# Kernel tuning notes

Hardware: AMD Instinct MI355X
Metric: run time of the kernel (lower is better)

Reference implementation:

```python
import math
import jax, jax.numpy as jnp
import numpy as np

HEAD_DIM = 128
SKETCH_DIM = 256  # multiple of 8, no padding needed in pack
_BIT_WEIGHTS = jnp.array([1, 2, 4, 8, 16, 32, 64, 128], dtype=jnp.uint8)


def _pack_bits(bits):
    # bits: uint8 0/1, trailing dim = SKETCH_DIM (multiple of 8)
    *lead, d = bits.shape
    b = bits.reshape(*lead, d // 8, 8)
    return (b * _BIT_WEIGHTS).sum(axis=-1).astype(jnp.uint8)


def _unpack_bits(packed, out_dim):
    # packed: uint8 [..., n] -> float32 [..., out_dim] of 0/1
    shifts = jnp.arange(8, dtype=jnp.uint8)
    bits = (packed[..., None] >> shifts) & jnp.uint8(1)
    bits = bits.reshape(*packed.shape[:-1], -1)[..., :out_dim]
    return bits.astype(jnp.float32)


def setup_inputs() -> dict:
    key = jax.random.key(0)
    kq, kk, kg = jax.random.split(key, 3)
    q = jax.random.normal(kq, (4, 32, 16, HEAD_DIM), dtype=jnp.float32)
    k = jax.random.normal(kk, (4, 32, 8192, HEAD_DIM), dtype=jnp.float32)
    G = jax.random.normal(kg, (HEAD_DIM, SKETCH_DIM), dtype=jnp.float32) / math.sqrt(SKETCH_DIM)
    return {"q": q, "k": k, "G": G}


def reference(q, k, G):
    # project_query: q @ G -> [B, H, Q, sketch_dim]
    q_sketch = jnp.einsum('bhqd,ds->bhqs', q, G)
    # sketch_key: sign-quantize k @ G, pack into uint8
    proj = jnp.einsum('bhkd,ds->bhks', k, G)
    bits = (proj > 0).astype(jnp.uint8)
    k_packed = _pack_bits(bits)  # [B, H, K, sketch_dim//8] uint8
    # estimate_scores: unpack to +/-1, dequant matmul, unbiasing scale
    k_signs = _unpack_bits(k_packed, SKETCH_DIM) * 2.0 - 1.0
    est = jnp.einsum('bhqs,bhks->bhqk', q_sketch, k_signs.astype(q_sketch.dtype))
    return est * jnp.float32(math.sqrt(math.pi / 2))
```

## Files before the change

### kernel.cpp

```cpp
#include <hip/hip_runtime.h>
#include <math.h>

typedef _Float16 f16;
typedef _Float16 f16x8 __attribute__((ext_vector_type(8)));
typedef float    f32x4 __attribute__((ext_vector_type(4)));
typedef unsigned int u32;
typedef unsigned long long u64;

#define NHEADS 128
#define KLEN   8192
#define DDIM   128
#define SDIM   256
#define NROWS  (NHEADS * KLEN)
#define SCALE  1.2533141373155003f
#define TAU    2e-5f

#define QS_OFF     0
#define GH_OFF     (1u << 20)
#define GL_OFF     ((1u << 20) + (64u << 10))
#define GT_OFF     ((1u << 20) + (128u << 10))
#define PACKED_OFF (2u << 20)

__device__ __forceinline__ float seq_dot_np(const float* __restrict__ a,
                                            const float* __restrict__ gcol) {
  float acc = 0.0f;
  #pragma unroll 8
  for (int d = 0; d < DDIM; ++d)
    acc = __builtin_fmaf(a[d], gcol[d], acc);
  return acc;
}

__global__ void prep_qs_kernel(const float* __restrict__ q,
                               const float* __restrict__ G,
                               f16* __restrict__ qs16) {
  int idx = blockIdx.x * 256 + threadIdx.x;
  int s  = idx & 255;
  int hq = idx >> 8;
  const float* qr = q + (size_t)hq * DDIM;
  float acc = 0.f;
  #pragma unroll 8
  for (int d = 0; d < DDIM; ++d) acc += qr[d] * G[d * SDIM + s];
  qs16[idx] = (f16)acc;
}

__global__ void prep_g_kernel(const float* __restrict__ G,
                              f16* __restrict__ gh, f16* __restrict__ gl,
                              float* __restrict__ gt) {
  int idx = blockIdx.x * 256 + threadIdx.x;
  int d = idx & 127;
  int s = idx >> 7;
  float g = G[d * SDIM + s];
  f16 h = (f16)g;
  gh[s * DDIM + d] = h;
  gl[s * DDIM + d] = (f16)((g - (float)h) * 4096.0f);
  gt[s * DDIM + d] = g;
}

__launch_bounds__(1024)
__global__ void proj_sign_kernel(const float* __restrict__ kmat,
                                 const f16* __restrict__ gh,
                                 const f16* __restrict__ gl,
                                 u32* __restrict__ packed,
                                 u32* __restrict__ smask) {
  __shared__ __align__(16) char smem[131072];

  const int tid  = threadIdx.x;
  const int lane = tid & 63;
  const int w    = tid >> 6;
  const int g4 = lane >> 4;
  const int ln = lane & 15;

  #pragma unroll
  for (int j = 0; j < 4; ++j) {
    int cidx = j * 1024 + tid;
    int s = cidx >> 4;
    int off = (cidx * 16) ^ ((s & 7) << 4);
    *(f16x8*)(smem + off)         = *(const f16x8*)(gh + (size_t)cidx * 8);
    *(f16x8*)(smem + 65536 + off) = *(const f16x8*)(gl + (size_t)cidx * 8);
  }
  __syncthreads();

  const int base = blockIdx.x * 512 + w * 32;

  f16x8 Ah[2][4], Al[2][4];
  #pragma unroll
  for (int rb = 0; rb < 2; ++rb) {
    const float* kr = kmat + (size_t)(base + rb * 16 + ln) * DDIM;
    #pragma unroll
    for (int c = 0; c < 4; ++c) {
      const float* p0 = kr + c * 32 + g4 * 8;
      float4 a0 = *(const float4*)p0;
      float4 a1 = *(const float4*)(p0 + 4);
      float af[8] = {a0.x, a0.y, a0.z, a0.w, a1.x, a1.y, a1.z, a1.w};
      f16x8 hh, ll;
      #pragma unroll
      for (int j = 0; j < 8; ++j) {
        f16 h = (f16)af[j];
        hh[j] = h;
        ll[j] = (f16)((af[j] - (float)h) * 4096.0f);
      }
      Ah[rb][c] = hh;
      Al[rb][c] = ll;
    }
  }

  u32 pw[2][8] = {{0}};
  u32 sw[2][8] = {{0}};

  #pragma unroll
  for (int tl = 0; tl < 16; ++tl) {
    const int s = tl * 16 + ln;
    const int sx = (s & 7) << 4;
    f16x8 Bh[4], Bl[4];
    #pragma unroll
    for (int c = 0; c < 4; ++c) {
      int off = (s * 256 + c * 64 + g4 * 16) ^ sx;
      Bh[c] = *(const f16x8*)(smem + off);
      Bl[c] = *(const f16x8*)(smem + 65536 + off);
    }
    f32x4 ah0 = {0,0,0,0}, aa0 = {0,0,0,0}, ab0 = {0,0,0,0};
    f32x4 ah1 = {0,0,0,0}, aa1 = {0,0,0,0}, ab1 = {0,0,0,0};
    #pragma unroll
    for (int c = 0; c < 4; ++c) {
      ah0 = __builtin_amdgcn_mfma_f32_16x16x32_f16(Ah[0][c], Bh[c], ah0, 0, 0, 0);
      aa0 = __builtin_amdgcn_mfma_f32_16x16x32_f16(Ah[0][c], Bl[c], aa0, 0, 0, 0);
      ab0 = __builtin_amdgcn_mfma_f32_16x16x32_f16(Al[0][c], Bh[c], ab0, 0, 0, 0);
      ah1 = __builtin_amdgcn_mfma_f32_16x16x32_f16(Ah[1][c], Bh[c], ah1, 0, 0, 0);
      aa1 = __builtin_amdgcn_mfma_f32_16x16x32_f16(Ah[1][c], Bl[c], aa1, 0, 0, 0);
      ab1 = __builtin_amdgcn_mfma_f32_16x16x32_f16(Al[1][c], Bh[c], ab1, 0, 0, 0);
    }
    float p[2][4];
    #pragma unroll
    for (int r = 0; r < 4; ++r) {
      p[0][r] = ah0[r] + (aa0[r] + ab0[r]) * 2.44140625e-4f;
      p[1][r] = ah1[r] + (aa1[r] + ab1[r]) * 2.44140625e-4f;
    }

    #pragma unroll
    for (int rb = 0; rb < 2; ++rb) {
      u64 b0 = __ballot(p[rb][0] > 0.0f ? 1 : 0);
      u64 b1 = __ballot(p[rb][1] > 0.0f ? 1 : 0);
      u64 b2 = __ballot(p[rb][2] > 0.0f ? 1 : 0);
      u64 b3 = __ballot(p[rb][3] > 0.0f ? 1 : 0);
      if (lane < 16) {
        int r = lane & 3;
        u64 b = (r == 0) ? b0 : (r == 1) ? b1 : (r == 2) ? b2 : b3;
        u32 sh = 16u * (u32)(lane >> 2);
        pw[rb][tl >> 1] |= ((u32)((b >> sh) & 0xffffu)) << (16 * (tl & 1));
      }
    }

    float mn = __builtin_fabsf(p[0][0]);
    #pragma unroll
    for (int rb = 0; rb < 2; ++rb)
      #pragma unroll
      for (int r = 0; r < 4; ++r)
        mn = fminf(mn, __builtin_fabsf(p[rb][r]));
    if (__any(mn < TAU ? 1 : 0)) {
      #pragma unroll
      for (int rb = 0; rb < 2; ++rb) {
        u64 t0 = __ballot(__builtin_fabsf(p[rb][0]) < TAU ? 1 : 0);
        u64 t1 = __ballot(__builtin_fabsf(p[rb][1]) < TAU ? 1 : 0);
        u64 t2 = __ballot(__builtin_fabsf(p[rb][2]) < TAU ? 1 : 0);
        u64 t3 = __ballot(__builtin_fabsf(p[rb][3]) < TAU ? 1 : 0);
        if (lane < 16) {
          int r = lane & 3;
          u64 t = (r == 0) ? t0 : (r == 1) ? t1 : (r == 2) ? t2 : t3;
          u32 sh = 16u * (u32)(lane >> 2);
          sw[rb][tl >> 1] |= ((u32)((t >> sh) & 0xffffu)) << (16 * (tl & 1));
        }
      }
    }
  }

  if (lane < 16) {
    #pragma unroll
    for (int rb = 0; rb < 2; ++rb) {
      size_t row = (size_t)(base + rb * 16 + lane);
      uint4 v0, v1, m0, m1;
      v0.x = pw[rb][0]; v0.y = pw[rb][1]; v0.z = pw[rb][2]; v0.w = pw[rb][3];
      v1.x = pw[rb][4]; v1.y = pw[rb][5]; v1.z = pw[rb][6]; v1.w = pw[rb][7];
      m0.x = sw[rb][0]; m0.y = sw[rb][1]; m0.z = sw[rb][2]; m0.w = sw[rb][3];
      m1.x = sw[rb][4]; m1.y = sw[rb][5]; m1.z = sw[rb][6]; m1.w = sw[rb][7];
      *(uint4*)(packed + row * 8)     = v0;
      *(uint4*)(packed + row * 8 + 4) = v1;
      *(uint4*)(smask  + row * 8)     = m0;
      *(uint4*)(smask  + row * 8 + 4) = m1;
    }
  }
}

__global__ void fixup_kernel(const float* __restrict__ kmat,
                             const float* __restrict__ gt,
                             u32* __restrict__ packed,
                             const u32* __restrict__ smask) {
  int row = blockIdx.x * 256 + threadIdx.x;
  if (row >= NROWS) return;
  const u32* mp = smask + (size_t)row * 8;
  uint4 m0 = *(const uint4*)mp;
  uint4 m1 = *(const uint4*)(mp + 4);
  u32 mw[8] = {m0.x, m0.y, m0.z, m0.w, m1.x, m1.y, m1.z, m1.w};
  if (!(mw[0] | mw[1] | mw[2] | mw[3] | mw[4] | mw[5] | mw[6] | mw[7])) return;
  const float* a = kmat + (size_t)row * DDIM;
  #pragma unroll
  for (int wd = 0; wd < 8; ++wd) {
    u32 m = mw[wd];
    if (!m) continue;
    u32 pk = packed[(size_t)row * 8 + wd];
    while (m) {
      int b = __ffs(m) - 1;  m &= m - 1;
      int s = wd * 32 + b;
      float acc = seq_dot_np(a, gt + (size_t)s * DDIM);
      if (acc > 0.0f) pk |= (1u << b);
      else            pk &= ~(1u << b);
    }
    packed[(size_t)row * 8 + wd] = pk;
  }
}

__launch_bounds__(256)
__global__ void est_kernel(const f16* __restrict__ qs16,
                           const u32* __restrict__ packed,
                           float* __restrict__ out) {
  const int tid  = threadIdx.x;
  const int lane = tid & 63;
  const int w    = tid >> 6;
  const int wg   = blockIdx.x;
  const int head   = wg >> 5;
  const int kchunk = (wg & 31) * 256;
  const int g4 = lane >> 4, ln = lane & 15;

  f16x8 aq[8];
  const f16* qb = qs16 + (size_t)head * 16 * SDIM;
  #pragma unroll
  for (int c = 0; c < 8; ++c)
    aq[c] = *(const f16x8*)(qb + ln * SDIM + c * 32 + g4 * 8);

  const int kb = kchunk + w * 64;
  #pragma unroll
  for (int kt = 0; kt < 4; ++kt) {
    int krow = kb + kt * 16 + ln;
    const u32* bp = packed + (size_t)(head * KLEN + krow) * 8;
    uint4 q0 = *(const uint4*)bp;
    uint4 q1 = *(const uint4*)(bp + 4);
    u32 b32[8] = {q0.x, q0.y, q0.z, q0.w, q1.x, q1.y, q1.z, q1.w};
    f32x4 acc = {0, 0, 0, 0};
    #pragma unroll
    for (int c = 0; c < 8; ++c) {
      u32 byte8 = (b32[c] >> (8 * g4)) & 0xffu;
      union { u32 u[4]; f16x8 h; } sv;
      #pragma unroll
      for (int pp = 0; pp < 4; ++pp) {
        u32 v = 0x3C003C00u;
        v |= ((byte8 >> (2 * pp))     & 1u) ? 0u : 0x8000u;
        v |= ((byte8 >> (2 * pp + 1)) & 1u) ? 0u : 0x80000000u;
        sv.u[pp] = v;
      }
      acc = __builtin_amdgcn_mfma_f32_16x16x32_f16(aq[c], sv.h, acc, 0, 0, 0);
    }
    float* ob = out + (size_t)(head * 16) * KLEN + kb + kt * 16 + ln;
    #pragma unroll
    for (int r = 0; r < 4; ++r) {
      int qrow = g4 * 4 + r;
      ob[(size_t)qrow * KLEN] = acc[r] * SCALE;
    }
  }
}

extern "C" void kernel_launch(void* const* d_in, const int* in_sizes, int n_in,
                              void* d_out, int out_size, void* d_ws, size_t ws_size,
                              hipStream_t stream) {
  const float* q = (const float*)d_in[0];
  const float* k = (const float*)d_in[1];
  const float* G = (const float*)d_in[2];
  float* out = (float*)d_out;
  char* ws = (char*)d_ws;

  f16*   qs16   = (f16*)(ws + QS_OFF);
  f16*   gh     = (f16*)(ws + GH_OFF);
  f16*   gl     = (f16*)(ws + GL_OFF);
  float* gt     = (float*)(ws + GT_OFF);
  u32*   packed = (u32*)(ws + PACKED_OFF);

  u32* smask = (u32*)d_out;

  prep_qs_kernel<<<2048, 256, 0, stream>>>(q, G, qs16);
  prep_g_kernel<<<128, 256, 0, stream>>>(G, gh, gl, gt);
  proj_sign_kernel<<<2048, 1024, 0, stream>>>(k, gh, gl, packed, smask);
  fixup_kernel<<<4096, 256, 0, stream>>>(k, gt, packed, smask);
  est_kernel<<<4096, 256, 0, stream>>>(qs16, packed, out);
}
```

Measured before the change: 363.4 us.

## Read MFMA-fragment-ordered G directly from global memory instead of shared memory

The G prep kernel now writes the f16 hi/lo split of G already laid out in per-lane MFMA fragment order, so the projection kernel loads B fragments straight from global memory (L1/L2-resident, 128 KB) with coalesced 16-byte loads. This removes the per-block 128 KB shared-memory staging and its barrier, so blocks shrink to 256 threads over 128 rows and the grid grows fourfold. The trade-off is that every wave re-reads G through the cache hierarchy instead of from LDS, which may add L2 traffic and latency.

```diff
diff --git a/kernel.cpp b/kernel.cpp
--- a/kernel.cpp
+++ b/kernel.cpp
@@ -16,8 +16,8 @@
 #define TAU    2e-5f
 
 #define QS_OFF     0
-#define GH_OFF     (1u << 20)
-#define GL_OFF     ((1u << 20) + (64u << 10))
+#define GFH_OFF    (1u << 20)
+#define GFL_OFF    ((1u << 20) + (64u << 10))
 #define GT_OFF     ((1u << 20) + (128u << 10))
 #define PACKED_OFF (2u << 20)
 
@@ -44,43 +44,40 @@
 }
 
 __global__ void prep_g_kernel(const float* __restrict__ G,
-                              f16* __restrict__ gh, f16* __restrict__ gl,
+                              f16* __restrict__ gfh, f16* __restrict__ gfl,
                               float* __restrict__ gt) {
-  int idx = blockIdx.x * 256 + threadIdx.x;
-  int d = idx & 127;
-  int s = idx >> 7;
-  float g = G[d * SDIM + s];
-  f16 h = (f16)g;
-  gh[s * DDIM + d] = h;
-  gl[s * DDIM + d] = (f16)((g - (float)h) * 4096.0f);
-  gt[s * DDIM + d] = g;
-}
-
-__launch_bounds__(1024)
+  int t = blockIdx.x * 256 + threadIdx.x;
+  int tl   = t >> 8;
+  int c    = (t >> 6) & 3;
+  int lane = t & 63;
+  int s  = tl * 16 + (lane & 15);
+  int d0 = c * 32 + (lane >> 4) * 8;
+  f16x8 hh, ll;
+  #pragma unroll
+  for (int j = 0; j < 8; ++j) {
+    float g = G[(size_t)(d0 + j) * SDIM + s];
+    f16 h = (f16)g;
+    hh[j] = h;
+    ll[j] = (f16)((g - (float)h) * 4096.0f);
+    gt[(size_t)s * DDIM + d0 + j] = g;
+  }
+  *(f16x8*)(gfh + (size_t)t * 8) = hh;
+  *(f16x8*)(gfl + (size_t)t * 8) = ll;
+}
+
+__launch_bounds__(256)
 __global__ void proj_sign_kernel(const float* __restrict__ kmat,
-                                 const f16* __restrict__ gh,
-                                 const f16* __restrict__ gl,
+                                 const f16* __restrict__ gfh,
+                                 const f16* __restrict__ gfl,
                                  u32* __restrict__ packed,
                                  u32* __restrict__ smask) {
-  __shared__ __align__(16) char smem[131072];
-
   const int tid  = threadIdx.x;
   const int lane = tid & 63;
   const int w    = tid >> 6;
   const int g4 = lane >> 4;
   const int ln = lane & 15;
 
-  #pragma unroll
-  for (int j = 0; j < 4; ++j) {
-    int cidx = j * 1024 + tid;
-    int s = cidx >> 4;
-    int off = (cidx * 16) ^ ((s & 7) << 4);
-    *(f16x8*)(smem + off)         = *(const f16x8*)(gh + (size_t)cidx * 8);
-    *(f16x8*)(smem + 65536 + off) = *(const f16x8*)(gl + (size_t)cidx * 8);
-  }
-  __syncthreads();
-
-  const int base = blockIdx.x * 512 + w * 32;
+  const int base = blockIdx.x * 128 + w * 32;
 
   f16x8 Ah[2][4], Al[2][4];
   #pragma unroll
@@ -107,16 +104,16 @@
   u32 pw[2][8] = {{0}};
   u32 sw[2][8] = {{0}};
 
+  const size_t loff = (size_t)lane * 8;
+
   #pragma unroll
   for (int tl = 0; tl < 16; ++tl) {
-    const int s = tl * 16 + ln;
-    const int sx = (s & 7) << 4;
     f16x8 Bh[4], Bl[4];
     #pragma unroll
     for (int c = 0; c < 4; ++c) {
-      int off = (s * 256 + c * 64 + g4 * 16) ^ sx;
-      Bh[c] = *(const f16x8*)(smem + off);
-      Bl[c] = *(const f16x8*)(smem + 65536 + off);
+      size_t o = (size_t)(tl * 4 + c) * 512 + loff;
+      Bh[c] = *(const f16x8*)(gfh + o);
+      Bl[c] = *(const f16x8*)(gfl + o);
     }
     f32x4 ah0 = {0,0,0,0}, aa0 = {0,0,0,0}, ab0 = {0,0,0,0};
     f32x4 ah1 = {0,0,0,0}, aa1 = {0,0,0,0}, ab1 = {0,0,0,0};
@@ -277,16 +274,16 @@
   char* ws = (char*)d_ws;
 
   f16*   qs16   = (f16*)(ws + QS_OFF);
-  f16*   gh     = (f16*)(ws + GH_OFF);
-  f16*   gl     = (f16*)(ws + GL_OFF);
+  f16*   gfh    = (f16*)(ws + GFH_OFF);
+  f16*   gfl    = (f16*)(ws + GFL_OFF);
   float* gt     = (float*)(ws + GT_OFF);
   u32*   packed = (u32*)(ws + PACKED_OFF);
 
   u32* smask = (u32*)d_out;
 
   prep_qs_kernel<<<2048, 256, 0, stream>>>(q, G, qs16);
-  prep_g_kernel<<<128, 256, 0, stream>>>(G, gh, gl, gt);
-  proj_sign_kernel<<<2048, 1024, 0, stream>>>(k, gh, gl, packed, smask);
+  prep_g_kernel<<<16, 256, 0, stream>>>(G, gfh, gfl, gt);
+  proj_sign_kernel<<<8192, 256, 0, stream>>>(k, gfh, gfl, packed, smask);
   fixup_kernel<<<4096, 256, 0, stream>>>(k, gt, packed, smask);
   est_kernel<<<4096, 256, 0, stream>>>(qs16, packed, out);
 }
```

New measurement: 371.5 us. 1.02x slower.
